# Kernel optimization log

Hardware: AMD Instinct MI355X
Metric: run time of the kernel (lower is better)

The kernel has to match this reference:

```python
import jax, jax.numpy as jnp
import numpy as np

B, S, E, H = 2, 2048, 2048, 16
HD = E // H  # head_dim = 128


def _rope(x):
    # x: (B, S, H, HD). Faithful to source: sin/cos built from head_dim,
    # but _rotate_every_two operates on the SEQUENCE axis (axis 1) and the
    # rearrange 'b d j ... -> b (d j) ...' with d=2 concatenates, not interleaves.
    s, hd = x.shape[1], x.shape[-1]
    inv_freq = 1.0 / 10000 ** (np.arange(0, hd, 2) / hd)          # (hd/2,)
    sinusoid = np.einsum('i,j->ij', np.arange(s), inv_freq)       # (s, hd/2)
    # einops.repeat 'b n -> b (n j)', j=2 interleaves each element twice
    sin = np.repeat(np.sin(sinusoid), 2, axis=1)[-s:, None, :]    # (s, 1, hd)
    cos = np.repeat(np.cos(sinusoid), 2, axis=1)[-s:, None, :]
    sin = jnp.asarray(sin, x.dtype)
    cos = jnp.asarray(cos, x.dtype)
    odds = x[:, 1::2]   # (B, S/2, H, HD)
    evens = x[:, ::2]
    rot = jnp.concatenate([-odds, evens], axis=1)  # (B, S, H, HD)
    return x * cos + rot * sin


def setup_inputs() -> dict:
    key = jax.random.key(0)
    k_in, kq, kk, kv, ko = jax.random.split(key, 5)
    scale_in = (1.0 / E) ** 0.5   # lecun_normal fan_in = E
    scale_out = (1.0 / E) ** 0.5  # out_proj fan_in = H*HD = E
    return {
        'inputs': jax.random.normal(k_in, (B, S, E), dtype=jnp.float32),
        'mask': jnp.zeros((1, 1, S, S), dtype=jnp.float32),
        'wq': jax.random.normal(kq, (E, H, HD), dtype=jnp.float32) * scale_in,
        'wk': jax.random.normal(kk, (E, H, HD), dtype=jnp.float32) * scale_in,
        'wv': jax.random.normal(kv, (E, H, HD), dtype=jnp.float32) * scale_in,
        'wo': jax.random.normal(ko, (H, HD, E), dtype=jnp.float32) * scale_out,
        'train': 0,
    }


def reference(inputs, mask, wq, wk, wv, wo, train):
    # QKV projections: (B,S,E) x (E,H,HD) -> (B,S,H,HD)
    q = jnp.einsum('bse,ehd->bshd', inputs, wq)
    k = jnp.einsum('bse,ehd->bshd', inputs, wk)
    v = jnp.einsum('bse,ehd->bshd', inputs, wv)
    q = _rope(q)
    k = _rope(k)
    # scores + custom norm: x / (2*hidden_dim)**(-0.5) == x * sqrt(2*E)
    norm_scale = (2.0 * E) ** 0.5
    qk = jnp.einsum('bshe,bShe->bhsS', q, k)
    attn = jax.nn.softmax((qk + mask) * norm_scale, axis=-1)
    self_attn = jnp.einsum('bhsS,bShe->bshe', attn, v)  # (B,S,H,HD)
    # out projection contracts (heads, kv): (B,S,H,HD) x (H,HD,E) -> (B,S,E)
    return jnp.einsum('bshd,hde->bse', self_attn, wo)
```

## Files before the change

### kernel.cpp

```cpp
#include <hip/hip_runtime.h>
#include <hip/hip_bf16.h>
#include <cmath>

#define Bn 2
#define Sn 2048
#define En 2048
#define Hn 16
#define HDn 128
#define Mn (Bn*Sn)
#define NORMS2 92.33248261689366f

typedef __attribute__((ext_vector_type(8))) short short8;
typedef __attribute__((ext_vector_type(4))) float f32x4;

__device__ __forceinline__ short f2bf(float x) {
    __hip_bfloat16 h = __float2bfloat16(x);
    return *reinterpret_cast<short*>(&h);
}
__device__ __forceinline__ float bf2f(short s) {
    __hip_bfloat16 h = *reinterpret_cast<__hip_bfloat16*>(&s);
    return __bfloat162float(h);
}
__device__ __forceinline__ void gl_lds16(const void* g, void* l) {
    __builtin_amdgcn_global_load_lds(
        (const __attribute__((address_space(1))) unsigned int*)g,
        (__attribute__((address_space(3))) unsigned int*)l, 16, 0, 0);
}

#if __has_builtin(__builtin_amdgcn_exp2f)
#define EXP2(x) __builtin_amdgcn_exp2f(x)
#else
#define EXP2(x) exp2f(x)
#endif

template<int CTRL>
__device__ __forceinline__ float dppf(float x) {
    int r = __builtin_amdgcn_update_dpp(0, __builtin_bit_cast(int, x), CTRL, 0xf, 0xf, true);
    return __builtin_bit_cast(float, r);
}
__device__ __forceinline__ float redmax16(float x) {
    x = fmaxf(x, dppf<0xB1>(x));
    x = fmaxf(x, dppf<0x4E>(x));
    x = fmaxf(x, dppf<0x141>(x));
    x = fmaxf(x, dppf<0x140>(x));
    return x;
}
__device__ __forceinline__ float redsum16(float x) {
    x += dppf<0xB1>(x);
    x += dppf<0x4E>(x);
    x += dppf<0x141>(x);
    x += dppf<0x140>(x);
    return x;
}

static __global__ void rope_table_kernel(float* __restrict__ sinT, float* __restrict__ cosT) {
    int i = blockIdx.x * 256 + threadIdx.x;
    int t = i >> 6, f = i & 63;
    double inv = pow(10000.0, -(double)(2 * f) / (double)HDn);
    double ang = (double)t * inv;
    sinT[i] = (float)sin(ang);
    cosT[i] = (float)cos(ang);
}

static __global__ void split_x_kernel(const float* __restrict__ X,
                                      short* __restrict__ Xhi, short* __restrict__ Xlo) {
    int i = (blockIdx.x * 256 + threadIdx.x) * 4;
    float4 x = *(const float4*)&X[i];
    short4 hi, lo;
    hi.x = f2bf(x.x); lo.x = f2bf(x.x - bf2f(hi.x));
    hi.y = f2bf(x.y); lo.y = f2bf(x.y - bf2f(hi.y));
    hi.z = f2bf(x.z); lo.z = f2bf(x.z - bf2f(hi.z));
    hi.w = f2bf(x.w); lo.w = f2bf(x.w - bf2f(hi.w));
    *(short4*)&Xhi[i] = hi;
    *(short4*)&Xlo[i] = lo;
}

static __global__ void maskconv_kernel(const float* __restrict__ M, short* __restrict__ MB) {
    int i = (blockIdx.x * 256 + threadIdx.x) * 4;
    float4 m = *(const float4*)&M[i];
    short4 o;
    o.x = f2bf(m.x * NORMS2); o.y = f2bf(m.y * NORMS2);
    o.z = f2bf(m.z * NORMS2); o.w = f2bf(m.w * NORMS2);
    *(short4*)&MB[i] = o;
}

static __global__ __launch_bounds__(256) void wtrans4_kernel(
        const float* __restrict__ Wq, const float* __restrict__ Wk,
        const float* __restrict__ Wv, const float* __restrict__ Wo,
        short* __restrict__ QKh, short* __restrict__ QKl,
        short* __restrict__ VT, short* __restrict__ OT) {
    __shared__ float tile[32][33];
    const int z = blockIdx.z;
    const float* W = (z == 0) ? Wq : (z == 1) ? Wk : (z == 2) ? Wv : Wo;
    short* Th = (z <= 1) ? QKh : (z == 2) ? VT : OT;
    const int rowoff = (z == 1) ? 2048 : 0;
    const bool split = (z <= 1);
    int tx = threadIdx.x & 31, ty = threadIdx.x >> 5;
    int k0 = blockIdx.y * 32, n0 = blockIdx.x * 32;
    #pragma unroll
    for (int i = 0; i < 4; ++i)
        tile[ty + i * 8][tx] = W[(size_t)(k0 + ty + i * 8) * En + n0 + tx];
    __syncthreads();
    #pragma unroll
    for (int i = 0; i < 4; ++i) {
        float v = tile[tx][ty + i * 8];
        size_t idx = (size_t)(rowoff + n0 + ty + i * 8) * En + k0 + tx;
        short hv = f2bf(v);
        Th[idx] = hv;
        if (split) QKl[idx] = f2bf(v - bf2f(hv));
    }
}

template<int NPROD, int OUTMODE>
static __global__ __launch_bounds__(256) void gemm_kernel(
        const short* __restrict__ Ahi, const short* __restrict__ Alo,
        const short* __restrict__ Bhi, const short* __restrict__ Blo,
        float* __restrict__ Cf, short* __restrict__ Cbt,
        int* __restrict__ Qpk, int* __restrict__ Kpk) {
    __shared__ short As_hi[2 * 128 * 32];
    __shared__ short Bs_hi[2 * 128 * 32];
    __shared__ short As_lo[NPROD == 3 ? 2 * 128 * 32 : 8];
    __shared__ short Bs_lo[NPROD == 3 ? 2 * 128 * 32 : 8];
    __shared__ short Ts[OUTMODE == 1 ? 128 * 136 : 8];

    const int tid = threadIdx.x;
    const int w = tid >> 6, l = tid & 63;
    const int quad = l >> 4, l15 = l & 15;
    const int wr = (w >> 1) * 64, wc = (w & 1) * 64;
    const int row0 = blockIdx.y * 128, col0 = blockIdx.x * 128;

    const int off0 = tid * 16;
    const int r_a = off0 >> 6;
    const int slot = (off0 >> 4) & 3;
    const int kb = (slot ^ ((r_a >> 1) & 3)) * 8;

    auto STAGE = [&](int bs, int kk) {
        const short* ap = Ahi + (size_t)(row0 + r_a) * En + kk + kb;
        const short* bp = Bhi + (size_t)(col0 + r_a) * En + kk + kb;
        gl_lds16(ap,           &As_hi[bs + off0 / 2]);
        gl_lds16(ap + 64 * En, &As_hi[bs + (off0 + 4096) / 2]);
        gl_lds16(bp,           &Bs_hi[bs + off0 / 2]);
        gl_lds16(bp + 64 * En, &Bs_hi[bs + (off0 + 4096) / 2]);
        if constexpr (NPROD == 3) {
            const short* ap2 = Alo + (size_t)(row0 + r_a) * En + kk + kb;
            const short* bp2 = Blo + (size_t)(col0 + r_a) * En + kk + kb;
            gl_lds16(ap2,           &As_lo[bs + off0 / 2]);
            gl_lds16(ap2 + 64 * En, &As_lo[bs + (off0 + 4096) / 2]);
            gl_lds16(bp2,           &Bs_lo[bs + off0 / 2]);
            gl_lds16(bp2 + 64 * En, &Bs_lo[bs + (off0 + 4096) / 2]);
        }
    };

    f32x4 acc[4][4];
    #pragma unroll
    for (int i = 0; i < 4; ++i)
        #pragma unroll
        for (int j = 0; j < 4; ++j) acc[i][j] = f32x4{0.f, 0.f, 0.f, 0.f};

    STAGE(0, 0);
    __syncthreads();

    for (int k0 = 0; k0 < En; k0 += 32) {
        const int cb = ((k0 >> 5) & 1) * 4096;
        const int nb = cb ^ 4096;
        if (k0 + 32 < En) {
            STAGE(nb, k0 + 32);
            asm volatile("s_waitcnt vmcnt(%0)" :: "i"(NPROD == 3 ? 8 : 4) : "memory");
        } else {
            asm volatile("s_waitcnt vmcnt(0)" ::: "memory");
        }
        __builtin_amdgcn_sched_barrier(0);
        __builtin_amdgcn_s_barrier();

        short8 bhf[4], blf[4];
        #pragma unroll
        for (int ni = 0; ni < 4; ++ni) {
            int br = wc + ni * 16 + l15;
            int bsw = (quad ^ ((br >> 1) & 3)) * 8;
            bhf[ni] = *(const short8*)&Bs_hi[cb + br * 32 + bsw];
            if constexpr (NPROD == 3)
                blf[ni] = *(const short8*)&Bs_lo[cb + br * 32 + bsw];
        }
        #pragma unroll
        for (int mi = 0; mi < 4; ++mi) {
            int ar = wr + mi * 16 + l15;
            int asw = (quad ^ ((ar >> 1) & 3)) * 8;
            short8 ahf = *(const short8*)&As_hi[cb + ar * 32 + asw];
            short8 alf;
            if constexpr (NPROD == 3)
                alf = *(const short8*)&As_lo[cb + ar * 32 + asw];
            #pragma unroll
            for (int ni = 0; ni < 4; ++ni) {
                acc[mi][ni] = __builtin_amdgcn_mfma_f32_16x16x32_bf16(ahf, bhf[ni], acc[mi][ni], 0, 0, 0);
                if constexpr (NPROD == 3) {
                    acc[mi][ni] = __builtin_amdgcn_mfma_f32_16x16x32_bf16(ahf, blf[ni], acc[mi][ni], 0, 0, 0);
                    acc[mi][ni] = __builtin_amdgcn_mfma_f32_16x16x32_bf16(alf, bhf[ni], acc[mi][ni], 0, 0, 0);
                }
            }
        }
        __builtin_amdgcn_s_barrier();
    }

    if constexpr (OUTMODE == 0) {
        #pragma unroll
        for (int mi = 0; mi < 4; ++mi)
            #pragma unroll
            for (int ni = 0; ni < 4; ++ni) {
                int r = row0 + wr + mi * 16 + quad * 4;
                int c = col0 + wc + ni * 16 + l15;
                #pragma unroll
                for (int reg = 0; reg < 4; ++reg)
                    Cf[(size_t)(r + reg) * En + c] = acc[mi][ni][reg];
            }
    } else if constexpr (OUTMODE == 1) {
        #pragma unroll
        for (int mi = 0; mi < 4; ++mi)
            #pragma unroll
            for (int ni = 0; ni < 4; ++ni) {
                int dl = wc + ni * 16 + l15;
                int sl = wr + mi * 16 + quad * 4;
                #pragma unroll
                for (int reg = 0; reg < 4; ++reg)
                    Ts[dl * 136 + sl + reg] = f2bf(acc[mi][ni][reg]);
            }
        __syncthreads();
        int dl = tid >> 1, s0 = (tid & 1) * 64;
        int b = row0 >> 11, h = col0 >> 7;
        size_t gbase = ((size_t)(b * Hn + h) * HDn + dl) * Sn + (row0 & (Sn - 1)) + s0;
        #pragma unroll
        for (int k = 0; k < 8; ++k) {
            short8 vv = *(const short8*)&Ts[dl * 136 + s0 + k * 8];
            *(short8*)&Cbt[gbase + k * 8] = vv;
        }
    } else {
        int* dst = (col0 >= 2048) ? Kpk : Qpk;
        const int cb = col0 & 2047;
        #pragma unroll
        for (int mi = 0; mi < 4; ++mi)
            #pragma unroll
            for (int ni = 0; ni < 4; ++ni) {
                int r = row0 + wr + mi * 16 + quad * 4;
                int c = cb + wc + ni * 16 + l15;
                #pragma unroll
                for (int reg = 0; reg < 4; ++reg) {
                    float v = acc[mi][ni][reg];
                    short hh = f2bf(v);
                    short ll = f2bf(v - bf2f(hh));
                    dst[(size_t)(r + reg) * 2048 + c] =
                        ((int)(unsigned short)hh << 16) | (unsigned short)ll;
                }
            }
    }
}

static __global__ void rope_pk_kernel(const int* __restrict__ Pre,
        short* __restrict__ Yh, short* __restrict__ Yl,
        const float* __restrict__ sinT, const float* __restrict__ cosT) {
    int p = blockIdx.x * 256 + threadIdx.x;
    int u = p & 511;
    int t = (p >> 9) & (Sn - 1);
    int b = p >> 20;
    int tsrc; float sgn;
    if (t < Sn / 2) { tsrc = 2 * t + 1; sgn = -1.f; }
    else            { tsrc = 2 * (t - Sn / 2); sgn = 1.f; }
    int f0 = (2 * u) & 63, f1 = (2 * u + 1) & 63;
    float sv0 = sinT[(t << 6) + f0], cv0 = cosT[(t << 6) + f0];
    float sv1 = sinT[(t << 6) + f1], cv1 = cosT[(t << 6) + f1];
    size_t rt = ((size_t)(b * Sn + t)) * 512 + u;
    size_t rs = ((size_t)(b * Sn + tsrc)) * 512 + u;
    int4 xt = ((const int4*)Pre)[rt];
    int4 xs = ((const int4*)Pre)[rs];
    auto up = [](int v) -> float {
        return bf2f((short)(v >> 16)) + bf2f((short)(v & 0xffff));
    };
    float x0 = up(xt.x), x1 = up(xt.y), x2 = up(xt.z), x3 = up(xt.w);
    float s0 = up(xs.x), s1 = up(xs.y), s2 = up(xs.z), s3 = up(xs.w);
    float y0 = x0 * cv0 + sgn * s0 * sv0;
    float y1 = x1 * cv0 + sgn * s1 * sv0;
    float y2 = x2 * cv1 + sgn * s2 * sv1;
    float y3 = x3 * cv1 + sgn * s3 * sv1;
    short4 hi, lo;
    hi.x = f2bf(y0); lo.x = f2bf(y0 - bf2f(hi.x));
    hi.y = f2bf(y1); lo.y = f2bf(y1 - bf2f(hi.y));
    hi.z = f2bf(y2); lo.z = f2bf(y2 - bf2f(hi.z));
    hi.w = f2bf(y3); lo.w = f2bf(y3 - bf2f(hi.w));
    size_t o = ((size_t)(b * Sn + t)) * En + 4 * u;
    *(short4*)&Yh[o] = hi;
    *(short4*)&Yl[o] = lo;
}

static __global__ __launch_bounds__(512, 2) void flash9_kernel(
        const short* __restrict__ Qhi, const short* __restrict__ Qlo,
        const short* __restrict__ Khi, const short* __restrict__ Klo,
        const short* __restrict__ Vt, const short* __restrict__ maskB,
        short* __restrict__ AO) {
    __shared__ short lds0[59392];

    const int tid = threadIdx.x;
    const int w = tid >> 6, l = tid & 63;
    const int quad = l >> 4, l15 = l & 15;
    const int n = blockIdx.x;
    const int bh = (n & 7) * 4 + ((n >> 3) & 3);
    const int qt = n >> 5;
    const int b = bh >> 4, h = bh & 15;
    const int r0 = qt * 128;
    const size_t qkbase = (size_t)b * Sn * En + (size_t)h * HDn;
    const int psb = 49152 + w * 1280;

    #pragma unroll
    for (int c = 0; c < 4; ++c) {
        int off = tid * 16 + c * 8192;
        int row = off >> 8;
        int gp = (off >> 4) & 15;
        int gl = gp ^ (row & 7);
        size_t gidx = qkbase + (size_t)(r0 + row) * En + gl * 8;
        gl_lds16(Qhi + gidx, &lds0[off / 2]);
        gl_lds16(Qlo + gidx, &lds0[16384 + off / 2]);
    }
    __syncthreads();
    short8 qh[4], ql[4];
    {
        int row = 16 * w + l15;
        #pragma unroll
        for (int kc = 0; kc < 4; ++kc) {
            int gp = (kc * 4 + quad) ^ (row & 7);
            qh[kc] = *(const short8*)&lds0[row * 128 + gp * 8];
            ql[kc] = *(const short8*)&lds0[16384 + row * 128 + gp * 8];
        }
    }
    __syncthreads();

    auto STAGE = [&](int bbase, int jj) {
        #pragma unroll
        for (int c = 0; c < 2; ++c) {
            int off = tid * 16 + c * 8192;
            int row = off >> 8;
            int gp = (off >> 4) & 15;
            int gl = gp ^ (row & 7);
            size_t gidx = qkbase + (size_t)(jj + row) * En + gl * 8;
            gl_lds16(Khi + gidx, &lds0[bbase + off / 2]);
            gl_lds16(Klo + gidx, &lds0[bbase + 8192 + off / 2]);
        }
        #pragma unroll
        for (int c = 0; c < 2; ++c) {
            int off = tid * 16 + c * 8192;
            int vrow = off >> 7;
            int vgp = (off >> 4) & 7;
            int vgl = vgp ^ (vrow & 7);
            size_t vidx = ((size_t)bh * HDn + vrow) * Sn + jj + vgl * 8;
            gl_lds16(Vt + vidx, &lds0[bbase + 16384 + off / 2]);
        }
    };

    STAGE(0, 0);
    __syncthreads();

    f32x4 O[8];
    #pragma unroll
    for (int di = 0; di < 8; ++di) O[di] = f32x4{0.f, 0.f, 0.f, 0.f};
    float m_prev[4] = {-INFINITY, -INFINITY, -INFINITY, -INFINITY};
    float l_run[4] = {0.f, 0.f, 0.f, 0.f};
    const int qrow_base = r0 + 16 * w + quad * 4;

    for (int j0 = 0; j0 < Sn; j0 += 64) {
        const int bb = ((j0 >> 6) & 1) * 24576;
        const int nb = bb ^ 24576;

        float mv[4][4];
        #pragma unroll
        for (int ni = 0; ni < 4; ++ni)
            #pragma unroll
            for (int reg = 0; reg < 4; ++reg)
                mv[ni][reg] = bf2f(maskB[(size_t)(qrow_base + reg) * Sn + j0 + ni * 16 + l15]);

        if (j0 + 64 < Sn) STAGE(nb, j0 + 64);

        f32x4 p[4];
        #pragma unroll
        for (int ni = 0; ni < 4; ++ni) p[ni] = f32x4{0.f, 0.f, 0.f, 0.f};
        #pragma unroll
        for (int ni = 0; ni < 4; ++ni) {
            int col = ni * 16 + l15;
            #pragma unroll
            for (int kc = 0; kc < 4; ++kc) {
                int gp = (kc * 4 + quad) ^ (col & 7);
                short8 kh = *(const short8*)&lds0[bb + col * 128 + gp * 8];
                short8 kl = *(const short8*)&lds0[bb + 8192 + col * 128 + gp * 8];
                p[ni] = __builtin_amdgcn_mfma_f32_16x16x32_bf16(qh[kc], kh, p[ni], 0, 0, 0);
                p[ni] = __builtin_amdgcn_mfma_f32_16x16x32_bf16(qh[kc], kl, p[ni], 0, 0, 0);
                p[ni] = __builtin_amdgcn_mfma_f32_16x16x32_bf16(ql[kc], kh, p[ni], 0, 0, 0);
            }
        }

        float rm[4] = {-INFINITY, -INFINITY, -INFINITY, -INFINITY};
        #pragma unroll
        for (int ni = 0; ni < 4; ++ni)
            #pragma unroll
            for (int reg = 0; reg < 4; ++reg) {
                float v = fmaf(p[ni][reg], NORMS2, mv[ni][reg]);
                p[ni][reg] = v;
                rm[reg] = fmaxf(rm[reg], v);
            }
        #pragma unroll
        for (int reg = 0; reg < 4; ++reg) rm[reg] = redmax16(rm[reg]);
        float al[4], mn[4], rs[4];
        #pragma unroll
        for (int reg = 0; reg < 4; ++reg) {
            mn[reg] = fmaxf(m_prev[reg], rm[reg]);
            al[reg] = EXP2(m_prev[reg] - mn[reg]);
            rs[reg] = 0.f;
        }
        #pragma unroll
        for (int ni = 0; ni < 4; ++ni)
            #pragma unroll
            for (int reg = 0; reg < 4; ++reg) {
                float pe = EXP2(p[ni][reg] - mn[reg]);
                rs[reg] += pe;
                lds0[psb + (quad * 4 + reg) * 80 + ((ni ^ quad) << 4) + l15] = f2bf(pe);
            }
        #pragma unroll
        for (int reg = 0; reg < 4; ++reg) rs[reg] = redsum16(rs[reg]);
        #pragma unroll
        for (int reg = 0; reg < 4; ++reg) {
            l_run[reg] = l_run[reg] * al[reg] + rs[reg];
            m_prev[reg] = mn[reg];
        }
        #pragma unroll
        for (int di = 0; di < 8; ++di)
            #pragma unroll
            for (int reg = 0; reg < 4; ++reg)
                O[di][reg] *= al[reg];

        short8 pa[2];
        #pragma unroll
        for (int kc2 = 0; kc2 < 2; ++kc2) {
            int g = kc2 * 2 + (quad >> 1);
            int gs = g ^ (l15 >> 2);
            pa[kc2] = *(const short8*)&lds0[psb + l15 * 80 + (gs << 4) + (quad & 1) * 8];
        }

        #pragma unroll
        for (int di = 0; di < 8; ++di) {
            int d = di * 16 + l15;
            #pragma unroll
            for (int kc2 = 0; kc2 < 2; ++kc2) {
                int gp = (kc2 * 4 + quad) ^ (d & 7);
                short8 vb = *(const short8*)&lds0[bb + 16384 + d * 64 + gp * 8];
                O[di] = __builtin_amdgcn_mfma_f32_16x16x32_bf16(pa[kc2], vb, O[di], 0, 0, 0);
            }
        }

        __syncthreads();
    }

    float inv[4];
    #pragma unroll
    for (int reg = 0; reg < 4; ++reg) inv[reg] = 1.0f / l_run[reg];
    #pragma unroll
    for (int di = 0; di < 8; ++di)
        #pragma unroll
        for (int reg = 0; reg < 4; ++reg) {
            size_t idx = ((size_t)b * Sn + qrow_base + reg) * En + h * HDn + di * 16 + l15;
            AO[idx] = f2bf(O[di][reg] * inv[reg]);
        }
}

extern "C" void kernel_launch(void* const* d_in, const int* in_sizes, int n_in,
                              void* d_out, int out_size, void* d_ws, size_t ws_size,
                              hipStream_t stream) {
    const float* inputs = (const float*)d_in[0];
    const float* mask   = (const float*)d_in[1];
    const float* wq     = (const float*)d_in[2];
    const float* wk     = (const float*)d_in[3];
    const float* wv     = (const float*)d_in[4];
    const float* wo     = (const float*)d_in[5];
    float* out = (float*)d_out;
    (void)in_sizes; (void)n_in; (void)out_size; (void)ws_size;

    char* W8 = (char*)d_ws;
    float* sinT  = (float*)(W8 + 0);
    float* cosT  = (float*)(W8 + 524288);
    short* Xhi   = (short*)(W8 + 1048576);
    short* Xlo   = (short*)(W8 + 17825792);
    short* maskB = (short*)(W8 + 34603008);
    short* WqkTh = (short*)(W8 + 42991616);
    short* WqkTl = (short*)(W8 + 59768832);
    short* WvT   = (short*)(W8 + 76546048);
    short* WoT   = (short*)(W8 + 84934656);
    int*   Qpk   = (int*)(W8 + 93323264);
    int*   Kpk   = (int*)(W8 + 126877696);
    short* Qhi = WqkTh;
    short* Qlo = WqkTl;
    short* Khi = (short*)(W8 + 93323264);
    short* Klo = (short*)(W8 + 110100480);
    short* Vt  = (short*)(W8 + 126877696);
    short* AO  = Xhi;

    rope_table_kernel<<<512, 256, 0, stream>>>(sinT, cosT);
    split_x_kernel<<<8192, 256, 0, stream>>>(inputs, Xhi, Xlo);
    maskconv_kernel<<<4096, 256, 0, stream>>>(mask, maskB);
    wtrans4_kernel<<<dim3(64, 64, 4), 256, 0, stream>>>(wq, wk, wv, wo,
                                                        WqkTh, WqkTl, WvT, WoT);

    gemm_kernel<3, 3><<<dim3(32, 32), 256, 0, stream>>>(
        Xhi, Xlo, WqkTh, WqkTl, nullptr, nullptr, Qpk, Kpk);
    rope_pk_kernel<<<8192, 256, 0, stream>>>(Qpk, Qhi, Qlo, sinT, cosT);
    rope_pk_kernel<<<8192, 256, 0, stream>>>(Kpk, Khi, Klo, sinT, cosT);
    gemm_kernel<1, 1><<<dim3(16, 32), 256, 0, stream>>>(
        Xhi, nullptr, WvT, nullptr, nullptr, Vt, nullptr, nullptr);

    flash9_kernel<<<512, 512, 0, stream>>>(Qhi, Qlo, Khi, Klo, Vt, maskB, AO);

    gemm_kernel<1, 0><<<dim3(16, 32), 256, 0, stream>>>(
        AO, nullptr, WoT, nullptr, out, nullptr, nullptr, nullptr);
}
```

Baseline: 648.2 us.

## Use 256x256 tiled 3-product split-bf16 GEMM for fused QK projection

Adds a dedicated gemm256 kernel with 512 threads and 256x256 output tiles for the Q/K projection, which uses the hi/lo split bf16 three-product MFMA scheme. Each wave now computes a 128x64 sub-tile, so every operand loaded into LDS feeds more MFMA work and global/LDS traffic per FLOP drops. The cost is much higher register pressure from 32 accumulators per lane and 128KB of LDS. The launch shrinks to 256 blocks, which risks lower occupancy and poorer load balance across CUs.

Result: faster. 620.0 us (-4.4%).

```diff
diff --git a/kernel.cpp b/kernel.cpp
--- a/kernel.cpp
+++ b/kernel.cpp
@@ -109,6 +109,105 @@
         Th[idx] = hv;
         if (split) QKl[idx] = f2bf(v - bf2f(hv));
     }
+}
+
+static __global__ __launch_bounds__(512, 2) void gemm256_kernel(
+        const short* __restrict__ Ahi, const short* __restrict__ Alo,
+        const short* __restrict__ Bhi, const short* __restrict__ Blo,
+        int* __restrict__ Qpk, int* __restrict__ Kpk) {
+    __shared__ short As_hi[2 * 256 * 32];
+    __shared__ short As_lo[2 * 256 * 32];
+    __shared__ short Bs_hi[2 * 256 * 32];
+    __shared__ short Bs_lo[2 * 256 * 32];
+
+    const int tid = threadIdx.x;
+    const int w = tid >> 6, l = tid & 63;
+    const int quad = l >> 4, l15 = l & 15;
+    const int wr = (w >> 2) * 128, wc = (w & 3) * 64;
+    const int row0 = blockIdx.y * 256, col0 = blockIdx.x * 256;
+
+    const int off0 = tid * 16;
+    const int r_a = off0 >> 6;
+    const int slot = (off0 >> 4) & 3;
+    const int kb = (slot ^ ((r_a >> 1) & 3)) * 8;
+
+    auto STAGE = [&](int bs, int kk) {
+        const short* ap  = Ahi + (size_t)(row0 + r_a) * En + kk + kb;
+        const short* bp  = Bhi + (size_t)(col0 + r_a) * En + kk + kb;
+        const short* ap2 = Alo + (size_t)(row0 + r_a) * En + kk + kb;
+        const short* bp2 = Blo + (size_t)(col0 + r_a) * En + kk + kb;
+        gl_lds16(ap,            &As_hi[bs + off0 / 2]);
+        gl_lds16(ap + 128 * En, &As_hi[bs + (off0 + 8192) / 2]);
+        gl_lds16(bp,            &Bs_hi[bs + off0 / 2]);
+        gl_lds16(bp + 128 * En, &Bs_hi[bs + (off0 + 8192) / 2]);
+        gl_lds16(ap2,            &As_lo[bs + off0 / 2]);
+        gl_lds16(ap2 + 128 * En, &As_lo[bs + (off0 + 8192) / 2]);
+        gl_lds16(bp2,            &Bs_lo[bs + off0 / 2]);
+        gl_lds16(bp2 + 128 * En, &Bs_lo[bs + (off0 + 8192) / 2]);
+    };
+
+    f32x4 acc[8][4];
+    #pragma unroll
+    for (int i = 0; i < 8; ++i)
+        #pragma unroll
+        for (int j = 0; j < 4; ++j) acc[i][j] = f32x4{0.f, 0.f, 0.f, 0.f};
+
+    STAGE(0, 0);
+    __syncthreads();
+
+    for (int k0 = 0; k0 < En; k0 += 32) {
+        const int cb = ((k0 >> 5) & 1) * 8192;
+        const int nb = cb ^ 8192;
+        if (k0 + 32 < En) {
+            STAGE(nb, k0 + 32);
+            asm volatile("s_waitcnt vmcnt(8)" ::: "memory");
+        } else {
+            asm volatile("s_waitcnt vmcnt(0)" ::: "memory");
+        }
+        __builtin_amdgcn_sched_barrier(0);
+        __builtin_amdgcn_s_barrier();
+
+        short8 bhf[4], blf[4];
+        #pragma unroll
+        for (int ni = 0; ni < 4; ++ni) {
+            int br = wc + ni * 16 + l15;
+            int bsw = (quad ^ ((br >> 1) & 3)) * 8;
+            bhf[ni] = *(const short8*)&Bs_hi[cb + br * 32 + bsw];
+            blf[ni] = *(const short8*)&Bs_lo[cb + br * 32 + bsw];
+        }
+        #pragma unroll
+        for (int mi = 0; mi < 8; ++mi) {
+            int ar = wr + mi * 16 + l15;
+            int asw = (quad ^ ((ar >> 1) & 3)) * 8;
+            short8 ahf = *(const short8*)&As_hi[cb + ar * 32 + asw];
+            short8 alf = *(const short8*)&As_lo[cb + ar * 32 + asw];
+            #pragma unroll
+            for (int ni = 0; ni < 4; ++ni) {
+                acc[mi][ni] = __builtin_amdgcn_mfma_f32_16x16x32_bf16(ahf, bhf[ni], acc[mi][ni], 0, 0, 0);
+                acc[mi][ni] = __builtin_amdgcn_mfma_f32_16x16x32_bf16(ahf, blf[ni], acc[mi][ni], 0, 0, 0);
+                acc[mi][ni] = __builtin_amdgcn_mfma_f32_16x16x32_bf16(alf, bhf[ni], acc[mi][ni], 0, 0, 0);
+            }
+        }
+        __builtin_amdgcn_s_barrier();
+    }
+
+    int* dst = (col0 >= 2048) ? Kpk : Qpk;
+    const int cbase = col0 & 2047;
+    #pragma unroll
+    for (int mi = 0; mi < 8; ++mi)
+        #pragma unroll
+        for (int ni = 0; ni < 4; ++ni) {
+            int r = row0 + wr + mi * 16 + quad * 4;
+            int c = cbase + wc + ni * 16 + l15;
+            #pragma unroll
+            for (int reg = 0; reg < 4; ++reg) {
+                float v = acc[mi][ni][reg];
+                short hh = f2bf(v);
+                short ll = f2bf(v - bf2f(hh));
+                dst[(size_t)(r + reg) * 2048 + c] =
+                    ((int)(unsigned short)hh << 16) | (unsigned short)ll;
+            }
+        }
 }
 
 template<int NPROD, int OUTMODE>
@@ -234,13 +333,13 @@
         }
     } else {
         int* dst = (col0 >= 2048) ? Kpk : Qpk;
-        const int cb = col0 & 2047;
+        const int cbx = col0 & 2047;
         #pragma unroll
         for (int mi = 0; mi < 4; ++mi)
             #pragma unroll
             for (int ni = 0; ni < 4; ++ni) {
                 int r = row0 + wr + mi * 16 + quad * 4;
-                int c = cb + wc + ni * 16 + l15;
+                int c = cbx + wc + ni * 16 + l15;
                 #pragma unroll
                 for (int reg = 0; reg < 4; ++reg) {
                     float v = acc[mi][ni][reg];
@@ -502,8 +601,8 @@
     wtrans4_kernel<<<dim3(64, 64, 4), 256, 0, stream>>>(wq, wk, wv, wo,
                                                         WqkTh, WqkTl, WvT, WoT);
 
-    gemm_kernel<3, 3><<<dim3(32, 32), 256, 0, stream>>>(
-        Xhi, Xlo, WqkTh, WqkTl, nullptr, nullptr, Qpk, Kpk);
+    gemm256_kernel<<<dim3(16, 16), 512, 0, stream>>>(
+        Xhi, Xlo, WqkTh, WqkTl, Qpk, Kpk);
     rope_pk_kernel<<<8192, 256, 0, stream>>>(Qpk, Qhi, Qlo, sinT, cosT);
     rope_pk_kernel<<<8192, 256, 0, stream>>>(Kpk, Khi, Klo, sinT, cosT);
     gemm_kernel<1, 1><<<dim3(16, 32), 256, 0, stream>>>(
```
